# Kernel optimization log

Measured on AMD Instinct MI355X. Metric: run time of the kernel, lower is better.

The kernel has to match this reference:

```python
import jax, jax.numpy as jnp
import numpy as np

B, N, D_U = 32, 4096, 64
D = 128          # mlp_dim == model dim after MLP
H = 2            # n_heads
DH = D // H


def setup_inputs() -> dict:
    key = jax.random.key(0)
    ks = jax.random.split(key, 16)
    sc = lambda fan_in: 1.0 / np.sqrt(fan_in)
    inp = {
        "u": jax.random.normal(ks[0], (B, N, D_U), dtype=jnp.float32),
        "x": jax.random.uniform(ks[1], (B, N, 2), dtype=jnp.float32),
        # MLP params: [D_U -> D -> D], gelu after each hidden layer
        "W1": jax.random.normal(ks[2], (D_U, D), dtype=jnp.float32) * sc(D_U),
        "b1": jnp.zeros((D,), jnp.float32),
        "W2": jax.random.normal(ks[3], (D, D), dtype=jnp.float32) * sc(D),
        "b2": jnp.zeros((D,), jnp.float32),
        # learned pooling query (nn.Embed(1, D))
        "embed": jax.random.normal(ks[4], (1, D), dtype=jnp.float32),
        # multihead linear attention projections
        "Wq": jax.random.normal(ks[5], (D, D), dtype=jnp.float32) * sc(D),
        "bq": jnp.zeros((D,), jnp.float32),
        "Wk": jax.random.normal(ks[6], (D, D), dtype=jnp.float32) * sc(D),
        "bk": jnp.zeros((D,), jnp.float32),
        "Wv": jax.random.normal(ks[7], (D, D), dtype=jnp.float32) * sc(D),
        "bv": jnp.zeros((D,), jnp.float32),
        "Wo": jax.random.normal(ks[8], (D, D), dtype=jnp.float32) * sc(D),
        "bo": jnp.zeros((D,), jnp.float32),
    }
    return inp


def reference(u, x, W1, b1, W2, b2, embed, Wq, bq, Wk, bk, Wv, bv, Wo, bo):
    # MLP on set elements: [B, N, D_U] -> [B, N, D]
    z = jax.nn.gelu(u @ W1 + b1)
    z = jax.nn.gelu(z @ W2 + b2)

    n = z.shape[1]
    # learned query broadcast over batch: [B, 1, D]
    s = jnp.broadcast_to(embed[None, :, :], (z.shape[0], 1, z.shape[-1]))

    # multihead linear (Galerkin-style, softmax-free) attention
    q = (s @ Wq + bq).reshape(z.shape[0], 1, H, DH)   # [B, 1, H, DH]
    k = (z @ Wk + bk).reshape(z.shape[0], n, H, DH)   # [B, N, H, DH]
    v = (z @ Wv + bv).reshape(z.shape[0], n, H, DH)   # [B, N, H, DH]

    # context = K^T V / N per head: [B, H, DH, DH]
    context = jnp.einsum("bnhd,bnhe->bhde", k, v) / n
    out = jnp.einsum("bqhd,bhde->bqhe", q, context)   # [B, 1, H, DH]
    out = out.reshape(z.shape[0], 1, D) @ Wo + bo     # [B, 1, D]

    return out[:, 0, :]                               # [B, D]
```

## Files before the change

kernel.cpp:

```cpp
#include <hip/hip_runtime.h>
#include <math.h>

#define Bsz 32
#define Nn  4096
#define DU  64
#define Dm  128

#define GRID_MLP 512

#define WS_WKQ 0
#define WS_BKQ 256
#define WS_CNT 288
#define WS_WP  8576
#define WS_M   20864
#define WS_VB  53632

#define H1STR 136

typedef short frag_ab __attribute__((ext_vector_type(8)));
typedef float frag_cd __attribute__((ext_vector_type(4)));

__device__ __forceinline__ unsigned short f2bf(float x) {
    union { float f; unsigned int u; } c; c.f = x;
    unsigned int r = c.u + 0x7fffu + ((c.u >> 16) & 1u);
    return (unsigned short)(r >> 16);
}

__device__ __forceinline__ unsigned int pk_bf16(float lo, float hi) {
    unsigned int r;
    asm("v_cvt_pk_bf16_f32 %0, %1, %2" : "=v"(r) : "v"(lo), "v"(hi));
    return r;
}

__device__ __forceinline__ float gelu_fast(float x) {
    float t = x * x;
    float a = x * fmaf(t, -0.1029432f, -2.3022081f);
    float e = __builtin_amdgcn_exp2f(a);
    return x * __builtin_amdgcn_rcpf(1.0f + e);
}

__global__ __launch_bounds__(256) void precompute_kernel(
    const float* __restrict__ embed, const float* __restrict__ Wq,
    const float* __restrict__ bq, const float* __restrict__ Wk,
    const float* __restrict__ bk, const float* __restrict__ W1,
    const float* __restrict__ W2, const float* __restrict__ Wv,
    const float* __restrict__ bv, const float* __restrict__ Wo,
    const float* __restrict__ bo, float* __restrict__ ws,
    float* __restrict__ out)
{
    __shared__ float qv[128];
    __shared__ float pp[256];
    const int tid = threadIdx.x;
    const int bid = blockIdx.x;

    if (bid < 12) {
        const int e = bid * 256 + tid;
        const int f = e >> 6, L = e & 63;
        const int q2 = L >> 4, n = L & 15;
        const float* src;
        int ks, nt;
        if (f < 16) { src = W1; ks = f >> 3;        nt = f & 7; }
        else        { src = W2; ks = (f - 16) >> 3; nt = (f - 16) & 7; }
        const int kb = ks * 32 + q2 * 8;
        const int c  = nt * 16 + n;
        unsigned int p[4];
        #pragma unroll
        for (int jj = 0; jj < 4; ++jj) {
            unsigned int lo = f2bf(src[(kb + 2 * jj)     * Dm + c]);
            unsigned int hi = f2bf(src[(kb + 2 * jj + 1) * Dm + c]);
            p[jj] = lo | (hi << 16);
        }
        ((uint4*)(ws + WS_WP))[e] = make_uint4(p[0], p[1], p[2], p[3]);
    } else if (bid == 12) {
        const int c = tid & 127, sg = tid >> 7;
        {
            float s = 0.f;
            #pragma unroll 8
            for (int j0 = 0; j0 < 64; ++j0) {
                const int j = sg * 64 + j0;
                s += embed[j] * Wq[j * 128 + c];
            }
            pp[tid] = s;
        }
        __syncthreads();
        if (tid < 128) qv[tid] = bq[tid] + pp[tid] + pp[128 + tid];
        __syncthreads();
        {
            float s = 0.f;
            #pragma unroll 8
            for (int dh = 0; dh < 64; ++dh)
                s += Wk[c * 128 + sg * 64 + dh] * qv[sg * 64 + dh];
            ws[WS_WKQ + sg * 128 + c] = s;
        }
        if (tid < 2) {
            float s = 0.f;
            for (int dh = 0; dh < 64; ++dh) s += bk[tid * 64 + dh] * qv[tid * 64 + dh];
            ws[WS_BKQ + tid] = s;
        }
    } else if (bid == 13) {
        for (int idx = WS_CNT + tid; idx < WS_WP; idx += 256) ws[idx] = 0.f;
    } else if (bid < 30) {
        const int base = (bid - 14) * 256 + tid;
        #pragma unroll
        for (int k = 0; k < 8; ++k) {
            const int o  = base + 4096 * k;
            const int hd = o >> 7, i = o & 127;
            const int h = hd >> 7, d = hd & 127;
            float acc = 0.f;
            #pragma unroll 8
            for (int c64 = 0; c64 < 64; ++c64)
                acc += Wv[d * 128 + h * 64 + c64] * Wo[(h * 64 + c64) * 128 + i];
            ws[WS_M + o] = acc * (1.0f / 4096.0f);
        }
    } else if (bid == 30) {
        if (tid < 256) {
            const int h = tid >> 7, i = tid & 127;
            float acc = 0.f;
            #pragma unroll 8
            for (int c64 = 0; c64 < 64; ++c64)
                acc += bv[h * 64 + c64] * Wo[(h * 64 + c64) * 128 + i];
            ws[WS_VB + tid] = acc * (1.0f / 4096.0f);
        }
    } else {
        for (int o = tid; o < Bsz * 128; o += 256) out[o] = bo[o & 127];
    }
}

__global__ __launch_bounds__(512) void mlp_pool_kernel(
    const float* __restrict__ u,  const float* __restrict__ b1,
    const float* __restrict__ b2, float* __restrict__ ws,
    float* __restrict__ out)
{
    __shared__ short lds_w[48 * 512];
    __shared__ short lds_h1[4 * 16 * H1STR];
    __shared__ float a2buf[4][16][2][2];
    __shared__ float b1_lds[128];

    const int tid  = threadIdx.x;
    const int wave = tid >> 6;
    const int lane = tid & 63;
    const int quad = lane >> 4;
    const int n15  = lane & 15;
    const int p    = wave >> 1;
    const int hf   = wave & 1;

    {
        const float4* src = (const float4*)(ws + WS_WP);
        float4* dst = (float4*)lds_w;
        #pragma unroll
        for (int i = 0; i < 6; ++i) dst[tid + 512 * i] = src[tid + 512 * i];
        if (tid < 128) b1_lds[tid] = b1[tid];
    }

    float b2c[4], wkq0[4], wkq1[4];
    #pragma unroll
    for (int nt = 0; nt < 4; ++nt) {
        const int c = hf * 64 + nt * 16 + n15;
        b2c[nt]  = b2[c];
        wkq0[nt] = ws[WS_WKQ + c];
        wkq1[nt] = ws[WS_WKQ + 128 + c];
    }
    const float bkq0 = ws[WS_BKQ];
    const float bkq1 = ws[WS_BKQ + 1];
    __syncthreads();

    const int bb = blockIdx.x >> 4;
    const int jb = blockIdx.x & 15;
    short* h1t = lds_h1 + p * 16 * H1STR;

    float s0p[4], s1p[4];
    #pragma unroll
    for (int nt = 0; nt < 4; ++nt) { s0p[nt] = 0.f; s1p[nt] = 0.f; }
    float aA0 = 0.f, aA1 = 0.f;

    const float* ub = u + ((size_t)(bb * Nn + jb * 256 + p * 16 + n15)) * DU + quad * 8;
    float4 f0 = *(const float4*)(ub);
    float4 f1 = *(const float4*)(ub + 4);
    float4 f2 = *(const float4*)(ub + 32);
    float4 f3 = *(const float4*)(ub + 36);

    #pragma unroll 1
    for (int it = 0; it < 4; ++it) {
        unsigned int ua[4], ub4[4];
        ua[0]  = pk_bf16(f0.x, f0.y); ua[1]  = pk_bf16(f0.z, f0.w);
        ua[2]  = pk_bf16(f1.x, f1.y); ua[3]  = pk_bf16(f1.z, f1.w);
        ub4[0] = pk_bf16(f2.x, f2.y); ub4[1] = pk_bf16(f2.z, f2.w);
        ub4[2] = pk_bf16(f3.x, f3.y); ub4[3] = pk_bf16(f3.z, f3.w);
        frag_ab a0 = *(const frag_ab*)ua;
        frag_ab a1 = *(const frag_ab*)ub4;

        #pragma unroll
        for (int i = 0; i < 4; ++i) {
            const int ct = hf * 4 + i;
            float4 bi = *(const float4*)&b1_lds[ct * 16 + quad * 4];
            frag_cd acc = (frag_cd){bi.x, bi.y, bi.z, bi.w};
            frag_ab w0 = *(const frag_ab*)&lds_w[(ct)     * 512 + lane * 8];
            acc = __builtin_amdgcn_mfma_f32_16x16x32_bf16(w0, a0, acc, 0, 0, 0);
            frag_ab w1 = *(const frag_ab*)&lds_w[(8 + ct) * 512 + lane * 8];
            acc = __builtin_amdgcn_mfma_f32_16x16x32_bf16(w1, a1, acc, 0, 0, 0);
            unsigned int lo = pk_bf16(gelu_fast(acc[0]), gelu_fast(acc[1]));
            unsigned int hi = pk_bf16(gelu_fast(acc[2]), gelu_fast(acc[3]));
            *(uint2*)&h1t[n15 * H1STR + ct * 16 + quad * 4] = make_uint2(lo, hi);
        }
        __syncthreads();

        if (it < 3) {
            const float* un = ub + (size_t)((it + 1) * 64) * DU;
            f0 = *(const float4*)(un);
            f1 = *(const float4*)(un + 4);
            f2 = *(const float4*)(un + 32);
            f3 = *(const float4*)(un + 36);
        }

        frag_cd acc2[4];
        #pragma unroll
        for (int nt = 0; nt < 4; ++nt)
            acc2[nt] = (frag_cd){b2c[nt], b2c[nt], b2c[nt], b2c[nt]};
        #pragma unroll
        for (int ks = 0; ks < 4; ++ks) {
            frag_ab a2 = *(const frag_ab*)&h1t[n15 * H1STR + ks * 32 + quad * 8];
            #pragma unroll
            for (int nt = 0; nt < 4; ++nt) {
                frag_ab w2f = *(const frag_ab*)&lds_w[(16 + ks * 8 + hf * 4 + nt) * 512 + lane * 8];
                acc2[nt] = __builtin_amdgcn_mfma_f32_16x16x32_bf16(a2, w2f, acc2[nt], 0, 0, 0);
            }
        }

        #pragma unroll
        for (int nt = 0; nt < 4; ++nt) {
            #pragma unroll
            for (int r = 0; r < 4; ++r)
                acc2[nt][r] = gelu_fast(acc2[nt][r]);
        }

        float p0[4], p1[4];
        #pragma unroll
        for (int r = 0; r < 4; ++r) { p0[r] = 0.f; p1[r] = 0.f; }
        #pragma unroll
        for (int nt = 0; nt < 4; ++nt) {
            #pragma unroll
            for (int r = 0; r < 4; ++r) {
                p0[r] += acc2[nt][r] * wkq0[nt];
                p1[r] += acc2[nt][r] * wkq1[nt];
            }
        }
        #pragma unroll
        for (int r = 0; r < 4; ++r) {
            #pragma unroll
            for (int d = 1; d < 16; d <<= 1) {
                p0[r] += __shfl_xor(p0[r], d);
                p1[r] += __shfl_xor(p1[r], d);
            }
        }
        if (n15 == 0) {
            #pragma unroll
            for (int r = 0; r < 4; ++r) {
                const int row = quad * 4 + r;
                a2buf[p][row][0][hf] = p0[r];
                a2buf[p][row][1][hf] = p1[r];
            }
        }
        __syncthreads();

        #pragma unroll
        for (int r = 0; r < 4; ++r) {
            const int row = quad * 4 + r;
            const float al0 = a2buf[p][row][0][0] + a2buf[p][row][0][1] + bkq0;
            const float al1 = a2buf[p][row][1][0] + a2buf[p][row][1][1] + bkq1;
            #pragma unroll
            for (int nt = 0; nt < 4; ++nt) {
                s0p[nt] += al0 * acc2[nt][r];
                s1p[nt] += al1 * acc2[nt][r];
            }
            aA0 += al0; aA1 += al1;
        }
    }

    #pragma unroll
    for (int nt = 0; nt < 4; ++nt) {
        s0p[nt] += __shfl_xor(s0p[nt], 16); s0p[nt] += __shfl_xor(s0p[nt], 32);
        s1p[nt] += __shfl_xor(s1p[nt], 16); s1p[nt] += __shfl_xor(s1p[nt], 32);
    }
    aA0 += __shfl_xor(aA0, 16); aA0 += __shfl_xor(aA0, 32);
    aA1 += __shfl_xor(aA1, 16); aA1 += __shfl_xor(aA1, 32);

    float* sw   = (float*)lds_h1;
    float* aw   = sw + 1024;
    float* Sb   = sw + 1032;
    float* part = sw + 1288;

    __syncthreads();

    if (quad == 0) {
        #pragma unroll
        for (int nt = 0; nt < 4; ++nt) {
            const int c = hf * 64 + nt * 16 + n15;
            sw[p * 256 + c]       = s0p[nt];
            sw[p * 256 + 128 + c] = s1p[nt];
        }
        if (hf == 0 && lane == 0) { aw[p * 2] = aA0; aw[p * 2 + 1] = aA1; }
    }
    __syncthreads();

    if (tid < 256)
        Sb[tid] = sw[tid] + sw[256 + tid] + sw[512 + tid] + sw[768 + tid];
    __syncthreads();

    {
        const int i = tid & 127, seg = tid >> 7;
        float acc = 0.f;
        #pragma unroll 8
        for (int k = 0; k < 64; ++k) {
            const int hd = seg * 64 + k;
            acc += Sb[hd] * ws[WS_M + hd * 128 + i];
        }
        part[tid] = acc;
    }
    __syncthreads();

    if (tid < 128) {
        const float aT0 = aw[0] + aw[2] + aw[4] + aw[6];
        const float aT1 = aw[1] + aw[3] + aw[5] + aw[7];
        atomicAdd(&out[bb * 128 + tid],
                  part[tid] + part[128 + tid] + part[256 + tid] + part[384 + tid]
                  + aT0 * ws[WS_VB + tid] + aT1 * ws[WS_VB + 128 + tid]);
    }
}

extern "C" void kernel_launch(void* const* d_in, const int* in_sizes, int n_in,
                              void* d_out, int out_size, void* d_ws, size_t ws_size,
                              hipStream_t stream) {
    const float* u     = (const float*)d_in[0];
    const float* W1    = (const float*)d_in[2];
    const float* b1    = (const float*)d_in[3];
    const float* W2    = (const float*)d_in[4];
    const float* b2    = (const float*)d_in[5];
    const float* embed = (const float*)d_in[6];
    const float* Wq    = (const float*)d_in[7];
    const float* bq    = (const float*)d_in[8];
    const float* Wk    = (const float*)d_in[9];
    const float* bk    = (const float*)d_in[10];
    const float* Wv    = (const float*)d_in[11];
    const float* bv    = (const float*)d_in[12];
    const float* Wo    = (const float*)d_in[13];
    const float* bo    = (const float*)d_in[14];
    float* ws  = (float*)d_ws;
    float* out = (float*)d_out;

    hipLaunchKernelGGL(precompute_kernel, dim3(32), dim3(256), 0, stream,
                       embed, Wq, bq, Wk, bk, W1, W2, Wv, bv, Wo, bo, ws, out);
    hipLaunchKernelGGL(mlp_pool_kernel, dim3(GRID_MLP), dim3(512), 0, stream,
                       u, b1, b2, ws, out);
}
```

Before: 131.4 us.

## Double-buffer h1 and alpha scratch to drop a barrier, read W1 from global

```diff
diff --git a/kernel.cpp b/kernel.cpp
--- a/kernel.cpp
+++ b/kernel.cpp
@@ -16,6 +16,8 @@
 #define WS_VB  53632
 
 #define H1STR 136
+#define H1TILE (16 * H1STR)
+#define H1BUF  (4 * H1TILE)
 
 typedef short frag_ab __attribute__((ext_vector_type(8)));
 typedef float frag_cd __attribute__((ext_vector_type(4)));
@@ -131,9 +133,9 @@
     const float* __restrict__ b2, float* __restrict__ ws,
     float* __restrict__ out)
 {
-    __shared__ short lds_w[48 * 512];
-    __shared__ short lds_h1[4 * 16 * H1STR];
-    __shared__ float a2buf[4][16][2][2];
+    __shared__ short lds_w2[32 * 512];
+    __shared__ short lds_h1[2 * H1BUF];
+    __shared__ float a2buf[2][4][16][2][2];
     __shared__ float b1_lds[128];
 
     const int tid  = threadIdx.x;
@@ -144,11 +146,12 @@
     const int p    = wave >> 1;
     const int hf   = wave & 1;
 
+    const uint4* wsrc = (const uint4*)(ws + WS_WP);
+
     {
-        const float4* src = (const float4*)(ws + WS_WP);
-        float4* dst = (float4*)lds_w;
-        #pragma unroll
-        for (int i = 0; i < 6; ++i) dst[tid + 512 * i] = src[tid + 512 * i];
+        uint4* dst = (uint4*)lds_w2;
+        #pragma unroll
+        for (int i = 0; i < 4; ++i) dst[tid + 512 * i] = wsrc[1024 + tid + 512 * i];
         if (tid < 128) b1_lds[tid] = b1[tid];
     }
 
@@ -166,12 +169,12 @@
 
     const int bb = blockIdx.x >> 4;
     const int jb = blockIdx.x & 15;
-    short* h1t = lds_h1 + p * 16 * H1STR;
 
     float s0p[4], s1p[4];
     #pragma unroll
     for (int nt = 0; nt < 4; ++nt) { s0p[nt] = 0.f; s1p[nt] = 0.f; }
     float aA0 = 0.f, aA1 = 0.f;
+    frag_cd acc2[4];
 
     const float* ub = u + ((size_t)(bb * Nn + jb * 256 + p * 16 + n15)) * DU + quad * 8;
     float4 f0 = *(const float4*)(ub);
@@ -189,18 +192,21 @@
         frag_ab a0 = *(const frag_ab*)ua;
         frag_ab a1 = *(const frag_ab*)ub4;
 
+        short* h1w = lds_h1 + (it & 1) * H1BUF + p * H1TILE;
+
         #pragma unroll
         for (int i = 0; i < 4; ++i) {
             const int ct = hf * 4 + i;
             float4 bi = *(const float4*)&b1_lds[ct * 16 + quad * 4];
             frag_cd acc = (frag_cd){bi.x, bi.y, bi.z, bi.w};
-            frag_ab w0 = *(const frag_ab*)&lds_w[(ct)     * 512 + lane * 8];
+            frag_ab w0 = *(const frag_ab*)&wsrc[(ct)     * 64 + lane];
             acc = __builtin_amdgcn_mfma_f32_16x16x32_bf16(w0, a0, acc, 0, 0, 0);
-            frag_ab w1 = *(const frag_ab*)&lds_w[(8 + ct) * 512 + lane * 8];
+            frag_ab w1 = *(const frag_ab*)&wsrc[(8 + ct) * 64 + lane];
             acc = __builtin_amdgcn_mfma_f32_16x16x32_bf16(w1, a1, acc, 0, 0, 0);
             unsigned int lo = pk_bf16(gelu_fast(acc[0]), gelu_fast(acc[1]));
             unsigned int hi = pk_bf16(gelu_fast(acc[2]), gelu_fast(acc[3]));
-            *(uint2*)&h1t[n15 * H1STR + ct * 16 + quad * 4] = make_uint2(lo, hi);
+            *(uint2*)&h1w[n15 * H1STR + ct * 16 + quad * 4] = make_uint2(lo, hi);
+            if (i == 1) __builtin_amdgcn_sched_barrier(0);
         }
         __syncthreads();
 
@@ -212,20 +218,34 @@
             f3 = *(const float4*)(un + 36);
         }
 
-        frag_cd acc2[4];
+        if (it > 0) {
+            const int pb = (it - 1) & 1;
+            #pragma unroll
+            for (int r = 0; r < 4; ++r) {
+                const int row = quad * 4 + r;
+                const float al0 = a2buf[pb][p][row][0][0] + a2buf[pb][p][row][0][1] + bkq0;
+                const float al1 = a2buf[pb][p][row][1][0] + a2buf[pb][p][row][1][1] + bkq1;
+                #pragma unroll
+                for (int nt = 0; nt < 4; ++nt) {
+                    s0p[nt] += al0 * acc2[nt][r];
+                    s1p[nt] += al1 * acc2[nt][r];
+                }
+                aA0 += al0; aA1 += al1;
+            }
+        }
+
         #pragma unroll
         for (int nt = 0; nt < 4; ++nt)
             acc2[nt] = (frag_cd){b2c[nt], b2c[nt], b2c[nt], b2c[nt]};
         #pragma unroll
         for (int ks = 0; ks < 4; ++ks) {
-            frag_ab a2 = *(const frag_ab*)&h1t[n15 * H1STR + ks * 32 + quad * 8];
+            frag_ab a2 = *(const frag_ab*)&h1w[n15 * H1STR + ks * 32 + quad * 8];
             #pragma unroll
             for (int nt = 0; nt < 4; ++nt) {
-                frag_ab w2f = *(const frag_ab*)&lds_w[(16 + ks * 8 + hf * 4 + nt) * 512 + lane * 8];
+                frag_ab w2f = *(const frag_ab*)&lds_w2[(ks * 8 + hf * 4 + nt) * 512 + lane * 8];
                 acc2[nt] = __builtin_amdgcn_mfma_f32_16x16x32_bf16(a2, w2f, acc2[nt], 0, 0, 0);
             }
         }
-
         #pragma unroll
         for (int nt = 0; nt < 4; ++nt) {
             #pragma unroll
@@ -256,17 +276,20 @@
             #pragma unroll
             for (int r = 0; r < 4; ++r) {
                 const int row = quad * 4 + r;
-                a2buf[p][row][0][hf] = p0[r];
-                a2buf[p][row][1][hf] = p1[r];
-            }
-        }
-        __syncthreads();
-
+                a2buf[it & 1][p][row][0][hf] = p0[r];
+                a2buf[it & 1][p][row][1][hf] = p1[r];
+            }
+        }
+    }
+
+    __syncthreads();
+
+    {
         #pragma unroll
         for (int r = 0; r < 4; ++r) {
             const int row = quad * 4 + r;
-            const float al0 = a2buf[p][row][0][0] + a2buf[p][row][0][1] + bkq0;
-            const float al1 = a2buf[p][row][1][0] + a2buf[p][row][1][1] + bkq1;
+            const float al0 = a2buf[1][p][row][0][0] + a2buf[1][p][row][0][1] + bkq0;
+            const float al1 = a2buf[1][p][row][1][0] + a2buf[1][p][row][1][1] + bkq1;
             #pragma unroll
             for (int nt = 0; nt < 4; ++nt) {
                 s0p[nt] += al0 * acc2[nt][r];
```

After: 139.5 us. 6.2% more time.
